# Optimization experiments

Hardware: AMD Instinct MI355X
Metric: run time of the kernel (lower is better)

## Reference

```python
import jax, jax.numpy as jnp
import numpy as np

D_MODEL = 1024
N_HEADS = 16
D_K = D_MODEL // N_HEADS
EPS = 1e-6


def setup_inputs() -> dict:
    key = jax.random.key(0)
    ks = jax.random.split(key, 11)
    s = 1.0 / np.sqrt(D_MODEL)
    return {
        "query": jax.random.normal(ks[0], (2, 8192, D_MODEL), jnp.float32),
        "key": jax.random.normal(ks[1], (2, 8192, D_MODEL), jnp.float32),
        "value": jax.random.normal(ks[2], (2, 8192, D_MODEL), jnp.float32),
        "wq": jax.random.normal(ks[3], (D_MODEL, D_MODEL), jnp.float32) * s,
        "bq": jax.random.normal(ks[4], (D_MODEL,), jnp.float32) * s,
        "wk": jax.random.normal(ks[5], (D_MODEL, D_MODEL), jnp.float32) * s,
        "bk": jax.random.normal(ks[6], (D_MODEL,), jnp.float32) * s,
        "wv": jax.random.normal(ks[7], (D_MODEL, D_MODEL), jnp.float32) * s,
        "bv": jax.random.normal(ks[8], (D_MODEL,), jnp.float32) * s,
        "wo": jax.random.normal(ks[9], (D_MODEL, D_MODEL), jnp.float32) * s,
        "bo": jax.random.normal(ks[10], (D_MODEL,), jnp.float32) * s,
    }


def _feature_map(x):
    # 'elu' feature map: elu(x) + 1
    return jax.nn.elu(x) + 1.0


def _split_heads(x, b, n):
    # [b, n, d_model] -> [b, h, n, d_k]
    return x.reshape(b, n, N_HEADS, D_K).transpose(0, 2, 1, 3)


def reference(query, key, value, wq, bq, wk, bk, wv, bv, wo, bo):
    b, n, _ = query.shape
    q = _split_heads(query @ wq.T + bq, b, n)
    k = _split_heads(key @ wk.T + bk, b, n)
    v = _split_heads(value @ wv.T + bv, b, n)
    q = _feature_map(q)
    k = _feature_map(k)
    # kv: [b,h,d_k,d_k] -- O(n) accumulation over sequence
    kv = jnp.einsum('bhnd,bhnm->bhdm', k, v)
    qkv = jnp.einsum('bhnd,bhdm->bhnm', q, kv)
    k_sum = k.sum(axis=2)                       # [b,h,d_k]
    normalizer = jnp.einsum('bhnd,bhd->bhn', q, k_sum)[..., None] + EPS
    out = qkv / normalizer                      # [b,h,n,d_k]
    out = out.transpose(0, 2, 1, 3).reshape(b, n, D_MODEL)
    out = out @ wo.T + bo
    return out
```

## Files before the change

kernel.cpp:

```cpp
#include <hip/hip_runtime.h>

#define DM 1024
#define NHEADS 16
#define DK 64
#define BSZ 2
#define NSEQ 8192
#define MROWS (BSZ*NSEQ)
#define NCHUNKS 16
#define CHUNKN 512

typedef unsigned short u16;
typedef __attribute__((ext_vector_type(8))) short short8;
typedef __attribute__((ext_vector_type(4))) float f32x4;

constexpr float EPS_F = 1e-6f;

__device__ __forceinline__ u16 f2bf(float x) {
  union { float f; unsigned u; } c; c.f = x;
  unsigned r = c.u + 0x7FFFu + ((c.u >> 16) & 1u);
  return (u16)(r >> 16);
}
__device__ __forceinline__ float bf2f(u16 h) {
  union { unsigned u; float f; } c; c.u = ((unsigned)h) << 16;
  return c.f;
}

typedef __attribute__((address_space(1))) const void gvoid_t;
typedef __attribute__((address_space(3))) void lvoid_t;
__device__ __forceinline__ void gl2lds16(const void* g, void* l) {
  __builtin_amdgcn_global_load_lds((gvoid_t*)g, (lvoid_t*)l, 16, 0, 0);
}

__global__ __launch_bounds__(256)
void split_kernel(const float* __restrict__ src, u16* __restrict__ hi,
                  u16* __restrict__ lo, int n4) {
  int i = blockIdx.x * 256 + threadIdx.x;
  const int stride = gridDim.x * 256;
  for (; i < n4; i += stride) {
    const float4 v = ((const float4*)src)[i];
    const u16 h0 = f2bf(v.x), h1 = f2bf(v.y), h2 = f2bf(v.z), h3 = f2bf(v.w);
    const u16 l0 = f2bf(v.x - bf2f(h0)), l1 = f2bf(v.y - bf2f(h1));
    const u16 l2 = f2bf(v.z - bf2f(h2)), l3 = f2bf(v.w - bf2f(h3));
    ((ushort4*)hi)[i] = make_ushort4(h0, h1, h2, h3);
    ((ushort4*)lo)[i] = make_ushort4(l0, l1, l2, l3);
  }
}

template<int ACT, int MODE>
__global__ __launch_bounds__(256)
void gemm_mfma_kernel(const u16* __restrict__ Ahi, const u16* __restrict__ Alo,
                      const u16* __restrict__ Whi, const u16* __restrict__ Wlo,
                      const float* __restrict__ bias, void* __restrict__ Cout,
                      float* __restrict__ ksum) {
  constexpr int K = DM, N = DM, BK = 32;
  __shared__ u16 Ash[128 * BK], Asl[128 * BK], Wsh[128 * BK], Wsl[128 * BK];
  const int tid = threadIdx.x;
  const int lane = tid & 63, wv = tid >> 6;
  const int bRow = blockIdx.y * 128, bCol = blockIdx.x * 128;

  const int s0 = wv * 128 + lane;
  const int s1 = s0 + 64;
  const int r0 = s0 >> 2, c0 = (s0 & 3) * 8;
  const int r1 = s1 >> 2, c1 = (s1 & 3) * 8;
  const u16* gAh0 = Ahi + (size_t)(bRow + r0) * K + c0;
  const u16* gAh1 = Ahi + (size_t)(bRow + r1) * K + c1;
  const u16* gAl0 = Alo + (size_t)(bRow + r0) * K + c0;
  const u16* gAl1 = Alo + (size_t)(bRow + r1) * K + c1;
  const u16* gWh0 = Whi + (size_t)(bCol + r0) * K + c0;
  const u16* gWh1 = Whi + (size_t)(bCol + r1) * K + c1;
  const u16* gWl0 = Wlo + (size_t)(bCol + r0) * K + c0;
  const u16* gWl1 = Wlo + (size_t)(bCol + r1) * K + c1;
  u16* const lA0 = Ash + (wv * 2 + 0) * 512;
  u16* const lA1 = Ash + (wv * 2 + 1) * 512;
  u16* const lB0 = Asl + (wv * 2 + 0) * 512;
  u16* const lB1 = Asl + (wv * 2 + 1) * 512;
  u16* const lC0 = Wsh + (wv * 2 + 0) * 512;
  u16* const lC1 = Wsh + (wv * 2 + 1) * 512;
  u16* const lD0 = Wsl + (wv * 2 + 0) * 512;
  u16* const lD1 = Wsl + (wv * 2 + 1) * 512;

  const int wm = (wv & 1) * 64, wn = (wv >> 1) * 64;
  const int fr = lane & 15, fk = (lane >> 4) * 8;

  f32x4 acc[4][4] = {};

  for (int k0 = 0; k0 < K; k0 += BK) {
    gl2lds16(gAh0 + k0, lA0); gl2lds16(gAh1 + k0, lA1);
    gl2lds16(gAl0 + k0, lB0); gl2lds16(gAl1 + k0, lB1);
    gl2lds16(gWh0 + k0, lC0); gl2lds16(gWh1 + k0, lC1);
    gl2lds16(gWl0 + k0, lD0); gl2lds16(gWl1 + k0, lD1);
    __syncthreads();

    short8 ah[4], al[4], bh[4], bl[4];
#pragma unroll
    for (int mt = 0; mt < 4; mt++) {
      ah[mt] = *(const short8*)(Ash + (wm + mt * 16 + fr) * BK + fk);
      al[mt] = *(const short8*)(Asl + (wm + mt * 16 + fr) * BK + fk);
    }
#pragma unroll
    for (int nt = 0; nt < 4; nt++) {
      bh[nt] = *(const short8*)(Wsh + (wn + nt * 16 + fr) * BK + fk);
      bl[nt] = *(const short8*)(Wsl + (wn + nt * 16 + fr) * BK + fk);
    }
#pragma unroll
    for (int mt = 0; mt < 4; mt++)
#pragma unroll
      for (int nt = 0; nt < 4; nt++) {
        acc[mt][nt] = __builtin_amdgcn_mfma_f32_16x16x32_bf16(ah[mt], bh[nt], acc[mt][nt], 0, 0, 0);
        acc[mt][nt] = __builtin_amdgcn_mfma_f32_16x16x32_bf16(ah[mt], bl[nt], acc[mt][nt], 0, 0, 0);
        acc[mt][nt] = __builtin_amdgcn_mfma_f32_16x16x32_bf16(al[mt], bh[nt], acc[mt][nt], 0, 0, 0);
      }
    __syncthreads();
  }

  const int erow = (lane >> 4) * 4;
  const int ecol = lane & 15;
  float bv[4];
#pragma unroll
  for (int nt = 0; nt < 4; nt++) bv[nt] = bias[bCol + wn + nt * 16 + ecol];
  float csum[4] = {0.f, 0.f, 0.f, 0.f};
#pragma unroll
  for (int mt = 0; mt < 4; mt++)
#pragma unroll
    for (int nt = 0; nt < 4; nt++)
#pragma unroll
      for (int r = 0; r < 4; r++) {
        const size_t row = (size_t)bRow + wm + mt * 16 + erow + r;
        const size_t col = (size_t)bCol + wn + nt * 16 + ecol;
        float v = acc[mt][nt][r] + bv[nt];
        if (ACT) v = v > 0.f ? (v + 1.f) : __expf(v);
        if (MODE == 0)      ((float*)Cout)[row * N + col] = v;
        else if (MODE == 1) ((u16*)Cout)[row * N + col] = f2bf(v);
        else {
          ((u16*)Cout)[col * (size_t)MROWS + row] = f2bf(v);
          if (MODE == 3) csum[nt] += v;
        }
      }
  if (MODE == 3) {
    const int bidx = bRow >> 13;
#pragma unroll
    for (int nt = 0; nt < 4; nt++) {
      float s = csum[nt];
      s += __shfl_xor(s, 16, 64);
      s += __shfl_xor(s, 32, 64);
      if ((lane >> 4) == 0)
        atomicAdd(&ksum[bidx * DM + bCol + wn + nt * 16 + ecol], s);
    }
  }
}

__global__ __launch_bounds__(256)
void kv_mfma_kernel(const u16* __restrict__ kT, const u16* __restrict__ vT,
                    float* __restrict__ part) {
  const int bh = blockIdx.y;
  const int b = bh >> 4, h = bh & 15;
  const size_t colbase = (size_t)b * NSEQ + blockIdx.x * CHUNKN;
  __shared__ u16 kts[64 * 64], vts[64 * 64];
  const int tid = threadIdx.x, lane = tid & 63, w = tid >> 6;
  const int wm = (w & 1) * 32, wd = (w >> 1) * 32;
  const int fr = lane & 15, fk = (lane >> 4) * 8;
  const int srow = lane >> 3, scol = (lane & 7) * 8;

  f32x4 acc[2][2] = {};

  for (int s = 0; s < CHUNKN / 64; s++) {
    const size_t cb = colbase + s * 64 + scol;
#pragma unroll
    for (int i = 0; i < 2; i++) {
      const int ii = w * 2 + i;
      const size_t grow = (size_t)(h * DK + ii * 8 + srow) * MROWS + cb;
      gl2lds16(vT + grow, vts + ii * 512);
      gl2lds16(kT + grow, kts + ii * 512);
    }
    __syncthreads();
#pragma unroll
    for (int ks = 0; ks < 2; ks++) {
      short8 af[2], bfr[2];
#pragma unroll
      for (int mt = 0; mt < 2; mt++)
        af[mt] = *(const short8*)(vts + (wm + mt * 16 + fr) * 64 + ks * 32 + fk);
#pragma unroll
      for (int dt = 0; dt < 2; dt++)
        bfr[dt] = *(const short8*)(kts + (wd + dt * 16 + fr) * 64 + ks * 32 + fk);
#pragma unroll
      for (int mt = 0; mt < 2; mt++)
#pragma unroll
        for (int dt = 0; dt < 2; dt++)
          acc[mt][dt] = __builtin_amdgcn_mfma_f32_16x16x32_bf16(af[mt], bfr[dt], acc[mt][dt], 0, 0, 0);
    }
    __syncthreads();
  }

  float* pp = part + ((size_t)blockIdx.x * 32 + bh) * (DK * DK);
  const int erow = (lane >> 4) * 4, ecol = lane & 15;
#pragma unroll
  for (int mt = 0; mt < 2; mt++)
#pragma unroll
    for (int dt = 0; dt < 2; dt++)
#pragma unroll
      for (int r = 0; r < 4; r++)
        pp[(wm + mt * 16 + erow + r) * DK + wd + dt * 16 + ecol] = acc[mt][dt][r];
}

__global__ __launch_bounds__(256)
void kvt_reduce_kernel(const float* __restrict__ part, u16* __restrict__ kvt) {
  const int bh = blockIdx.x, t = threadIdx.x;
  const int i0 = t * 16;
  f32x4 s[4] = {};
  for (int c = 0; c < NCHUNKS; c++) {
    const f32x4* p = (const f32x4*)(part + ((size_t)c * 32 + bh) * (DK * DK) + i0);
#pragma unroll
    for (int q = 0; q < 4; q++) s[q] += p[q];
  }
  short8 o[2];
#pragma unroll
  for (int j = 0; j < 16; j++) o[j >> 3][j & 7] = (short)f2bf(s[j >> 2][j & 3]);
  *(short8*)(kvt + (size_t)bh * (DK * DK) + i0) = o[0];
  *(short8*)(kvt + (size_t)bh * (DK * DK) + i0 + 8) = o[1];
}

__global__ __launch_bounds__(256)
void attn_mfma_kernel(const u16* __restrict__ qp, const u16* __restrict__ kvt,
                      const float* __restrict__ ksum,
                      u16* __restrict__ ahi, u16* __restrict__ alo) {
  const int bh = blockIdx.y;
  const int b = bh >> 4, h = bh & 15;
  const int n0 = blockIdx.x * 128;
  const int tid = threadIdx.x, lane = tid & 63, w = tid >> 6;
  const int fr = lane & 15, fk = (lane >> 4) * 8;
  __shared__ float norm_lds[128];

  short8 bfr[4][2];
#pragma unroll
  for (int mt = 0; mt < 4; mt++)
#pragma unroll
    for (int ks = 0; ks < 2; ks++)
      bfr[mt][ks] = *(const short8*)(kvt + (size_t)bh * (DK * DK) + (mt * 16 + fr) * DK + ks * 32 + fk);

  float ksf[2][8];
#pragma unroll
  for (int ks = 0; ks < 2; ks++)
#pragma unroll
    for (int j = 0; j < 8; j++)
      ksf[ks][j] = ksum[b * DM + h * DK + ks * 32 + fk + j];

  const int nb = n0 + w * 32;
  short8 af[2][2];
#pragma unroll
  for (int nt = 0; nt < 2; nt++)
#pragma unroll
    for (int ks = 0; ks < 2; ks++)
      af[nt][ks] = *(const short8*)(qp + (size_t)(b * NSEQ + nb + nt * 16 + fr) * DM + h * DK + ks * 32 + fk);

  f32x4 acc[2][4] = {};
#pragma unroll
  for (int nt = 0; nt < 2; nt++)
#pragma unroll
    for (int mt = 0; mt < 4; mt++)
#pragma unroll
      for (int ks = 0; ks < 2; ks++)
        acc[nt][mt] = __builtin_amdgcn_mfma_f32_16x16x32_bf16(af[nt][ks], bfr[mt][ks], acc[nt][mt], 0, 0, 0);

#pragma unroll
  for (int nt = 0; nt < 2; nt++) {
    float p = 0.f;
#pragma unroll
    for (int ks = 0; ks < 2; ks++)
#pragma unroll
      for (int j = 0; j < 8; j++)
        p += bf2f((u16)af[nt][ks][j]) * ksf[ks][j];
    p += __shfl_xor(p, 16, 64);
    p += __shfl_xor(p, 32, 64);
    if ((lane >> 4) == 0) norm_lds[w * 32 + nt * 16 + fr] = p + EPS_F;
  }
  __syncthreads();

  const int erow = (lane >> 4) * 4, ec = lane & 15;
#pragma unroll
  for (int nt = 0; nt < 2; nt++) {
    float inv[4];
#pragma unroll
    for (int r = 0; r < 4; r++) inv[r] = 1.f / norm_lds[w * 32 + nt * 16 + erow + r];
#pragma unroll
    for (int mt = 0; mt < 4; mt++)
#pragma unroll
      for (int r = 0; r < 4; r++) {
        const float v = acc[nt][mt][r] * inv[r];
        const size_t o = (size_t)(b * NSEQ + nb + nt * 16 + erow + r) * DM + h * DK + mt * 16 + ec;
        const u16 hh = f2bf(v);
        ahi[o] = hh;
        alo[o] = f2bf(v - bf2f(hh));
      }
  }
}

extern "C" void kernel_launch(void* const* d_in, const int* in_sizes, int n_in,
                              void* d_out, int out_size, void* d_ws, size_t ws_size,
                              hipStream_t stream) {
  const float* query = (const float*)d_in[0];
  const float* key   = (const float*)d_in[1];
  const float* value = (const float*)d_in[2];
  const float* wq = (const float*)d_in[3];
  const float* bq = (const float*)d_in[4];
  const float* wk = (const float*)d_in[5];
  const float* bk = (const float*)d_in[6];
  const float* wv = (const float*)d_in[7];
  const float* bv = (const float*)d_in[8];
  const float* wo = (const float*)d_in[9];
  const float* bo = (const float*)d_in[10];
  float* out = (float*)d_out;

  constexpr size_t WELEM = (size_t)DM * DM;
  constexpr size_t AELEM = (size_t)MROWS * DM;

  char* p = (char*)d_ws;
  auto take = [&](size_t bytes) { char* q = p; p += (bytes + 255) & ~(size_t)255; return q; };
  u16* wqh = (u16*)take(WELEM * 2); u16* wql = (u16*)take(WELEM * 2);
  u16* wkh = (u16*)take(WELEM * 2); u16* wkl = (u16*)take(WELEM * 2);
  u16* wvh = (u16*)take(WELEM * 2); u16* wvl = (u16*)take(WELEM * 2);
  u16* woh = (u16*)take(WELEM * 2); u16* wol = (u16*)take(WELEM * 2);
  u16* chi = (u16*)take(AELEM * 2); u16* clo = (u16*)take(AELEM * 2);
  u16* qp  = (u16*)take(AELEM * 2);
  u16* kT  = (u16*)take(AELEM * 2);
  u16* vT  = (u16*)take(AELEM * 2);
  float* part = (float*)take((size_t)NCHUNKS * 32 * DK * DK * 4);
  float* ksum = (float*)take((size_t)BSZ * DM * 4);
  u16* kvt = (u16*)take((size_t)BSZ * NHEADS * DK * DK * 2);
  u16* ahi = chi; u16* alo = clo;

  hipMemsetAsync(ksum, 0, (size_t)BSZ * DM * 4, stream);

  const dim3 blk(256);
  split_kernel<<<256, blk, 0, stream>>>(wq, wqh, wql, (int)(WELEM / 4));
  split_kernel<<<256, blk, 0, stream>>>(wk, wkh, wkl, (int)(WELEM / 4));
  split_kernel<<<256, blk, 0, stream>>>(wv, wvh, wvl, (int)(WELEM / 4));
  split_kernel<<<256, blk, 0, stream>>>(wo, woh, wol, (int)(WELEM / 4));

  const dim3 ggrid(DM / 128, MROWS / 128);
  split_kernel<<<2048, blk, 0, stream>>>(query, chi, clo, (int)(AELEM / 4));
  gemm_mfma_kernel<1, 1><<<ggrid, blk, 0, stream>>>(chi, clo, wqh, wql, bq, qp, nullptr);
  split_kernel<<<2048, blk, 0, stream>>>(key, chi, clo, (int)(AELEM / 4));
  gemm_mfma_kernel<1, 3><<<ggrid, blk, 0, stream>>>(chi, clo, wkh, wkl, bk, kT, ksum);
  split_kernel<<<2048, blk, 0, stream>>>(value, chi, clo, (int)(AELEM / 4));
  gemm_mfma_kernel<0, 2><<<ggrid, blk, 0, stream>>>(chi, clo, wvh, wvl, bv, vT, nullptr);

  kv_mfma_kernel<<<dim3(NCHUNKS, BSZ * NHEADS), blk, 0, stream>>>(kT, vT, part);
  kvt_reduce_kernel<<<32, blk, 0, stream>>>(part, kvt);
  attn_mfma_kernel<<<dim3(NSEQ / 128, BSZ * NHEADS), blk, 0, stream>>>(qp, kvt, ksum, ahi, alo);
  gemm_mfma_kernel<0, 0><<<ggrid, blk, 0, stream>>>(ahi, alo, woh, wol, bo, out, nullptr);
}
```

Before: 778.8 us.

## Use 32x32x16 MFMA tiles in GEMM, vectorize transposed stores, merge weight splits

```diff
diff --git a/kernel.cpp b/kernel.cpp
--- a/kernel.cpp
+++ b/kernel.cpp
@@ -12,6 +12,7 @@
 typedef unsigned short u16;
 typedef __attribute__((ext_vector_type(8))) short short8;
 typedef __attribute__((ext_vector_type(4))) float f32x4;
+typedef __attribute__((ext_vector_type(16))) float f32x16;
 
 constexpr float EPS_F = 1e-6f;
 
@@ -43,6 +44,29 @@
     const u16 l2 = f2bf(v.z - bf2f(h2)), l3 = f2bf(v.w - bf2f(h3));
     ((ushort4*)hi)[i] = make_ushort4(h0, h1, h2, h3);
     ((ushort4*)lo)[i] = make_ushort4(l0, l1, l2, l3);
+  }
+}
+
+__global__ __launch_bounds__(256)
+void wsplit_kernel(const float* __restrict__ w0, const float* __restrict__ w1,
+                   const float* __restrict__ w2, const float* __restrict__ w3,
+                   u16* __restrict__ h0, u16* __restrict__ l0,
+                   u16* __restrict__ h1, u16* __restrict__ l1,
+                   u16* __restrict__ h2, u16* __restrict__ l2,
+                   u16* __restrict__ h3, u16* __restrict__ l3) {
+  constexpr int per = DM * DM / 4;
+  int i = blockIdx.x * 256 + threadIdx.x;
+  const int stride = gridDim.x * 256;
+  for (; i < 4 * per; i += stride) {
+    const int w = i >> 18, j = i & (per - 1);
+    const float* src = w == 0 ? w0 : w == 1 ? w1 : w == 2 ? w2 : w3;
+    u16* hi = w == 0 ? h0 : w == 1 ? h1 : w == 2 ? h2 : h3;
+    u16* lo = w == 0 ? l0 : w == 1 ? l1 : w == 2 ? l2 : l3;
+    const float4 v = ((const float4*)src)[j];
+    const u16 a0 = f2bf(v.x), a1 = f2bf(v.y), a2 = f2bf(v.z), a3 = f2bf(v.w);
+    ((ushort4*)hi)[j] = make_ushort4(a0, a1, a2, a3);
+    ((ushort4*)lo)[j] = make_ushort4(f2bf(v.x - bf2f(a0)), f2bf(v.y - bf2f(a1)),
+                                     f2bf(v.z - bf2f(a2)), f2bf(v.w - bf2f(a3)));
   }
 }
 
@@ -80,9 +104,9 @@
   u16* const lD1 = Wsl + (wv * 2 + 1) * 512;
 
   const int wm = (wv & 1) * 64, wn = (wv >> 1) * 64;
-  const int fr = lane & 15, fk = (lane >> 4) * 8;
-
-  f32x4 acc[4][4] = {};
+  const int fr = lane & 31, fk = (lane >> 5) * 8;
+
+  f32x16 acc[2][2] = {};
 
   for (int k0 = 0; k0 < K; k0 += BK) {
     gl2lds16(gAh0 + k0, lA0); gl2lds16(gAh1 + k0, lA1);
@@ -91,60 +115,80 @@
     gl2lds16(gWl0 + k0, lD0); gl2lds16(gWl1 + k0, lD1);
     __syncthreads();
 
-    short8 ah[4], al[4], bh[4], bl[4];
-#pragma unroll
-    for (int mt = 0; mt < 4; mt++) {
-      ah[mt] = *(const short8*)(Ash + (wm + mt * 16 + fr) * BK + fk);
-      al[mt] = *(const short8*)(Asl + (wm + mt * 16 + fr) * BK + fk);
-    }
-#pragma unroll
-    for (int nt = 0; nt < 4; nt++) {
-      bh[nt] = *(const short8*)(Wsh + (wn + nt * 16 + fr) * BK + fk);
-      bl[nt] = *(const short8*)(Wsl + (wn + nt * 16 + fr) * BK + fk);
-    }
-#pragma unroll
-    for (int mt = 0; mt < 4; mt++)
-#pragma unroll
-      for (int nt = 0; nt < 4; nt++) {
-        acc[mt][nt] = __builtin_amdgcn_mfma_f32_16x16x32_bf16(ah[mt], bh[nt], acc[mt][nt], 0, 0, 0);
-        acc[mt][nt] = __builtin_amdgcn_mfma_f32_16x16x32_bf16(ah[mt], bl[nt], acc[mt][nt], 0, 0, 0);
-        acc[mt][nt] = __builtin_amdgcn_mfma_f32_16x16x32_bf16(al[mt], bh[nt], acc[mt][nt], 0, 0, 0);
+    short8 ah[2][2], al[2][2], bh[2][2], bl[2][2];
+#pragma unroll
+    for (int mt = 0; mt < 2; mt++)
+#pragma unroll
+      for (int ks = 0; ks < 2; ks++) {
+        ah[mt][ks] = *(const short8*)(Ash + (wm + mt * 32 + fr) * BK + ks * 16 + fk);
+        al[mt][ks] = *(const short8*)(Asl + (wm + mt * 32 + fr) * BK + ks * 16 + fk);
       }
+#pragma unroll
+    for (int nt = 0; nt < 2; nt++)
+#pragma unroll
+      for (int ks = 0; ks < 2; ks++) {
+        bh[nt][ks] = *(const short8*)(Wsh + (wn + nt * 32 + fr) * BK + ks * 16 + fk);
+        bl[nt][ks] = *(const short8*)(Wsl + (wn + nt * 32 + fr) * BK + ks * 16 + fk);
+      }
+#pragma unroll
+    for (int ks = 0; ks < 2; ks++)
+#pragma unroll
+      for (int mt = 0; mt < 2; mt++)
+#pragma unroll
+        for (int nt = 0; nt < 2; nt++) {
+          acc[mt][nt] = __builtin_amdgcn_mfma_f32_32x32x16_bf16(ah[mt][ks], bh[nt][ks], acc[mt][nt], 0, 0, 0);
+          acc[mt][nt] = __builtin_amdgcn_mfma_f32_32x32x16_bf16(ah[mt][ks], bl[nt][ks], acc[mt][nt], 0, 0, 0);
+          acc[mt][nt] = __builtin_amdgcn_mfma_f32_32x32x16_bf16(al[mt][ks], bh[nt][ks], acc[mt][nt], 0, 0, 0);
+        }
     __syncthreads();
   }
 
-  const int erow = (lane >> 4) * 4;
-  const int ecol = lane & 15;
-  float bv[4];
-#pragma unroll
-  for (int nt = 0; nt < 4; nt++) bv[nt] = bias[bCol + wn + nt * 16 + ecol];
-  float csum[4] = {0.f, 0.f, 0.f, 0.f};
-#pragma unroll
-  for (int mt = 0; mt < 4; mt++)
-#pragma unroll
-    for (int nt = 0; nt < 4; nt++)
-#pragma unroll
-      for (int r = 0; r < 4; r++) {
-        const size_t row = (size_t)bRow + wm + mt * 16 + erow + r;
-        const size_t col = (size_t)bCol + wn + nt * 16 + ecol;
-        float v = acc[mt][nt][r] + bv[nt];
-        if (ACT) v = v > 0.f ? (v + 1.f) : __expf(v);
-        if (MODE == 0)      ((float*)Cout)[row * N + col] = v;
-        else if (MODE == 1) ((u16*)Cout)[row * N + col] = f2bf(v);
-        else {
-          ((u16*)Cout)[col * (size_t)MROWS + row] = f2bf(v);
-          if (MODE == 3) csum[nt] += v;
+  const int rhalf = (lane >> 5) * 4;
+  const int ec = lane & 31;
+  float bv[2];
+#pragma unroll
+  for (int nt = 0; nt < 2; nt++) bv[nt] = bias[bCol + wn + nt * 32 + ec];
+  float csum[2] = {0.f, 0.f};
+#pragma unroll
+  for (int mt = 0; mt < 2; mt++)
+#pragma unroll
+    for (int nt = 0; nt < 2; nt++) {
+      if (MODE >= 2) {
+        const size_t colg = (size_t)(bCol + wn + nt * 32 + ec);
+#pragma unroll
+        for (int q = 0; q < 4; q++) {
+          ushort4 o4;
+          u16* o = (u16*)&o4;
+#pragma unroll
+          for (int rr = 0; rr < 4; rr++) {
+            float v = acc[mt][nt][q * 4 + rr] + bv[nt];
+            if (ACT) v = v > 0.f ? (v + 1.f) : __expf(v);
+            if (MODE == 3) csum[nt] += v;
+            o[rr] = f2bf(v);
+          }
+          const size_t rowb = (size_t)bRow + wm + mt * 32 + 8 * q + rhalf;
+          *(ushort4*)((u16*)Cout + colg * MROWS + rowb) = o4;
+        }
+      } else {
+#pragma unroll
+        for (int r = 0; r < 16; r++) {
+          const size_t row = (size_t)bRow + wm + mt * 32 + (r & 3) + 8 * (r >> 2) + rhalf;
+          const size_t col = (size_t)bCol + wn + nt * 32 + ec;
+          float v = acc[mt][nt][r] + bv[nt];
+          if (ACT) v = v > 0.f ? (v + 1.f) : __expf(v);
+          if (MODE == 0) ((float*)Cout)[row * N + col] = v;
+          else           ((u16*)Cout)[row * N + col] = f2bf(v);
         }
       }
+    }
   if (MODE == 3) {
     const int bidx = bRow >> 13;
 #pragma unroll
-    for (int nt = 0; nt < 4; nt++) {
+    for (int nt = 0; nt < 2; nt++) {
       float s = csum[nt];
-      s += __shfl_xor(s, 16, 64);
       s += __shfl_xor(s, 32, 64);
-      if ((lane >> 4) == 0)
-        atomicAdd(&ksum[bidx * DM + bCol + wn + nt * 16 + ecol], s);
+      if (lane < 32)
+        atomicAdd(&ksum[bidx * DM + bCol + wn + nt * 32 + lane], s);
     }
   }
 }
@@ -331,10 +375,8 @@
   hipMemsetAsync(ksum, 0, (size_t)BSZ * DM * 4, stream);
 
   const dim3 blk(256);
-  split_kernel<<<256, blk, 0, stream>>>(wq, wqh, wql, (int)(WELEM / 4));
-  split_kernel<<<256, blk, 0, stream>>>(wk, wkh, wkl, (int)(WELEM / 4));
-  split_kernel<<<256, blk, 0, stream>>>(wv, wvh, wvl, (int)(WELEM / 4));
-  split_kernel<<<256, blk, 0, stream>>>(wo, woh, wol, (int)(WELEM / 4));
+  wsplit_kernel<<<1024, blk, 0, stream>>>(wq, wk, wv, wo, wqh, wql, wkh, wkl,
+                                          wvh, wvl, woh, wol);
 
   const dim3 ggrid(DM / 128, MROWS / 128);
   split_kernel<<<2048, blk, 0, stream>>>(query, chi, clo, (int)(AELEM / 4));
```

Measured after the change: 807.6 us. 3.7% more time.
